# Kernel tuning notes

Measured on AMD Instinct MI355X. Metric: run time of the kernel, lower is better.

## Reference

```python
import jax, jax.numpy as jnp
import numpy as np

N_NODES = 50000
N_EDGES = 800000
IN_CH, HID_CH, OUT_CH = 512, 128, 64


def gcn_conv(x, W, b, src, dst, num_nodes):
    """PyG GCNConv: add self-loops, sym-normalize, linear, scatter-add, bias.
    x: [N, Fin], W: [Fout, Fin], b: [Fout], src/dst: [E] int."""
    loop = jnp.arange(num_nodes, dtype=src.dtype)
    src2 = jnp.concatenate([src, loop])  # [E+N]
    dst2 = jnp.concatenate([dst, loop])
    deg = jax.ops.segment_sum(jnp.ones_like(dst2, dtype=x.dtype), dst2,
                              num_segments=num_nodes)  # in-degree + 1
    d_inv_sqrt = jnp.where(deg > 0, jax.lax.rsqrt(deg), 0.0)
    norm = d_inv_sqrt[src2] * d_inv_sqrt[dst2]  # [E+N]
    h = x @ W.T  # [N, Fout]
    msg = h[src2] * norm[:, None]  # [E+N, Fout] -- dominant memory traffic
    out = jax.ops.segment_sum(msg, dst2, num_segments=num_nodes)
    return out + b


def setup_inputs() -> dict:
    key = jax.random.key(0)
    ks = jax.random.split(key, 8)
    x = jax.random.normal(ks[0], (N_NODES, IN_CH), dtype=jnp.float32)
    edge_index = jax.random.randint(ks[1], (2, N_EDGES), 0, N_NODES, dtype=jnp.int64)
    s1 = 1.0 / np.sqrt(IN_CH)
    s2 = 1.0 / np.sqrt(HID_CH)
    W1 = jax.random.normal(ks[2], (HID_CH, IN_CH), dtype=jnp.float32) * s1
    b1 = jnp.zeros((HID_CH,), dtype=jnp.float32)
    W_mu = jax.random.normal(ks[3], (OUT_CH, HID_CH), dtype=jnp.float32) * s2
    b_mu = jnp.zeros((OUT_CH,), dtype=jnp.float32)
    W_logstd = jax.random.normal(ks[4], (OUT_CH, HID_CH), dtype=jnp.float32) * s2
    b_logstd = jnp.zeros((OUT_CH,), dtype=jnp.float32)
    return {"x": x, "edge_index": edge_index, "W1": W1, "b1": b1,
            "W_mu": W_mu, "b_mu": b_mu, "W_logstd": W_logstd, "b_logstd": b_logstd}


def reference(x, edge_index, W1, b1, W_mu, b_mu, W_logstd, b_logstd):
    src, dst = edge_index[0], edge_index[1]
    n = x.shape[0]
    h = jax.nn.relu(gcn_conv(x, W1, b1, src, dst, n))
    mu = gcn_conv(h, W_mu, b_mu, src, dst, n)
    logstd = gcn_conv(h, W_logstd, b_logstd, src, dst, n)
    return (mu, logstd)
```

## Files before the change

kernel.cpp:

```cpp
#include <hip/hip_runtime.h>

constexpr int FIN = 512;
constexpr int FH  = 128;
constexpr int FO  = 64;

typedef short short8 __attribute__((ext_vector_type(8)));
typedef float f32x4 __attribute__((ext_vector_type(4)));

__device__ __forceinline__ unsigned short f2bf(float f) {
    unsigned u = __float_as_uint(f);
    u += 0x7fffu + ((u >> 16) & 1u);
    return (unsigned short)(u >> 16);
}
__device__ __forceinline__ float bf2f(unsigned short h) {
    return __uint_as_float((unsigned)h << 16);
}


__global__ void convw1_kernel(const float* __restrict__ W, unsigned short* __restrict__ Wb,
                              int n4) {
    int i = blockIdx.x * blockDim.x + threadIdx.x;
    if (i < n4) {
        float4 v = ((const float4*)W)[i];
        ushort4 p;
        p.x = f2bf(v.x); p.y = f2bf(v.y); p.z = f2bf(v.z); p.w = f2bf(v.w);
        ((ushort4*)Wb)[i] = p;
    }
}

__global__ void convw2_kernel(const float* __restrict__ Wmu, const float* __restrict__ Wlg,
                              unsigned short* __restrict__ Wh, unsigned short* __restrict__ Wl) {
    int i = blockIdx.x * blockDim.x + threadIdx.x;
    if (i < 128 * 128) {
        int r = i >> 7, c = i & 127;
        float f = (r < 64) ? Wmu[r * 128 + c] : Wlg[(r - 64) * 128 + c];
        unsigned short h = f2bf(f);
        Wh[i] = h;
        Wl[i] = f2bf(f - bf2f(h));
    }
}


__global__ void count_kernel(const int* __restrict__ dst, int* __restrict__ cnt, int E) {
    int i = blockIdx.x * blockDim.x + threadIdx.x;
    if (i < E) atomicAdd(&cnt[dst[i]], 1);
}

__global__ void dinv_kernel(const int* __restrict__ cnt, float* __restrict__ dinv, int n) {
    int i = blockIdx.x * blockDim.x + threadIdx.x;
    if (i < n) dinv[i] = rsqrtf((float)(cnt[i] + 1));
}


__global__ void scan1_kernel(const int* __restrict__ cnt, int* __restrict__ offs,
                             int* __restrict__ bsum, int n) {
    __shared__ int sdata[256];
    int t = threadIdx.x;
    int base = blockIdx.x * 1024 + t * 4;
    int4 c = make_int4(0, 0, 0, 0);
    if (base + 3 < n) {
        c = *(const int4*)(cnt + base);
    } else {
        if (base + 0 < n) c.x = cnt[base + 0];
        if (base + 1 < n) c.y = cnt[base + 1];
        if (base + 2 < n) c.z = cnt[base + 2];
        if (base + 3 < n) c.w = cnt[base + 3];
    }
    int s0 = c.x + c.y + c.z + c.w;
    sdata[t] = s0;
    __syncthreads();
    for (int off = 1; off < 256; off <<= 1) {
        int v = (t >= off) ? sdata[t - off] : 0;
        __syncthreads();
        sdata[t] += v;
        __syncthreads();
    }
    int excl = sdata[t] - s0;
    if (t == 255) bsum[blockIdx.x] = sdata[255];
    if (base + 0 < n) offs[base + 0] = excl;
    if (base + 1 < n) offs[base + 1] = excl + c.x;
    if (base + 2 < n) offs[base + 2] = excl + c.x + c.y;
    if (base + 3 < n) offs[base + 3] = excl + c.x + c.y + c.z;
}

__global__ void scan2_kernel(int* __restrict__ bsum, int nb) {
    __shared__ int sdata[256];
    int t = threadIdx.x;
    int v = (t < nb) ? bsum[t] : 0;
    sdata[t] = v;
    __syncthreads();
    for (int off = 1; off < 256; off <<= 1) {
        int u = (t >= off) ? sdata[t - off] : 0;
        __syncthreads();
        sdata[t] += u;
        __syncthreads();
    }
    if (t < nb) bsum[t] = sdata[t] - v;
}

__global__ void scan3_kernel(int* __restrict__ offs, const int* __restrict__ bsum,
                             int n, int E) {
    int i = blockIdx.x * blockDim.x + threadIdx.x;
    if (i < n) offs[i] += bsum[i >> 10];
    if (i == 0) offs[n] = E;
}


__global__ void fill_kernel(const int* __restrict__ src, const int* __restrict__ dst,
                            const float* __restrict__ dinv, const int* __restrict__ offs,
                            int* __restrict__ cursor, int2* __restrict__ esort, int E) {
    int i = blockIdx.x * blockDim.x + threadIdx.x;
    if (i < E) {
        int s = src[i];
        int d = dst[i];
        int pos = offs[d] + atomicAdd(&cursor[d], 1);
        float w = dinv[s] * dinv[d];
        esort[pos] = make_int2(s, __float_as_int(w));
    }
}


__global__ void spmm_kernel(const unsigned int* __restrict__ hin, const int* __restrict__ offs,
                            const int2* __restrict__ esort, const float* __restrict__ dinv,
                            const float* __restrict__ bias, unsigned int* __restrict__ hout,
                            int n, int relu) {
    int gid = blockIdx.x * blockDim.x + threadIdx.x;
    int node = gid >> 6;
    int lane = threadIdx.x & 63;
    if (node >= n) return;
    float di = dinv[node];
    unsigned hv = hin[(size_t)node * 64 + lane];
    float ax = di * di * __uint_as_float(hv << 16);
    float ay = di * di * __uint_as_float(hv & 0xffff0000u);
    int p = offs[node];
    int end = offs[node + 1];
    for (; p + 4 <= end; p += 4) {
        int2 e0 = esort[p + 0];
        int2 e1 = esort[p + 1];
        int2 e2 = esort[p + 2];
        int2 e3 = esort[p + 3];
        unsigned v0 = hin[(size_t)e0.x * 64 + lane];
        unsigned v1 = hin[(size_t)e1.x * 64 + lane];
        unsigned v2 = hin[(size_t)e2.x * 64 + lane];
        unsigned v3 = hin[(size_t)e3.x * 64 + lane];
        float w0 = __int_as_float(e0.y), w1 = __int_as_float(e1.y);
        float w2 = __int_as_float(e2.y), w3 = __int_as_float(e3.y);
        ax = fmaf(w0, __uint_as_float(v0 << 16), ax);
        ay = fmaf(w0, __uint_as_float(v0 & 0xffff0000u), ay);
        ax = fmaf(w1, __uint_as_float(v1 << 16), ax);
        ay = fmaf(w1, __uint_as_float(v1 & 0xffff0000u), ay);
        ax = fmaf(w2, __uint_as_float(v2 << 16), ax);
        ay = fmaf(w2, __uint_as_float(v2 & 0xffff0000u), ay);
        ax = fmaf(w3, __uint_as_float(v3 << 16), ax);
        ay = fmaf(w3, __uint_as_float(v3 & 0xffff0000u), ay);
    }
    for (; p < end; ++p) {
        int2 e = esort[p];
        unsigned v = hin[(size_t)e.x * 64 + lane];
        float w = __int_as_float(e.y);
        ax = fmaf(w, __uint_as_float(v << 16), ax);
        ay = fmaf(w, __uint_as_float(v & 0xffff0000u), ay);
    }
    if (bias) {
        float2 b = ((const float2*)bias)[lane];
        ax += b.x; ay += b.y;
    }
    if (relu) { ax = fmaxf(ax, 0.f); ay = fmaxf(ay, 0.f); }
    unsigned o = (unsigned)f2bf(ax) | ((unsigned)f2bf(ay) << 16);
    hout[(size_t)node * 64 + lane] = o;
}


__global__ __launch_bounds__(256, 3) void gemm1_kernel(
    const float* __restrict__ X, const unsigned short* __restrict__ Wb,
    unsigned short* __restrict__ out, int M) {
    __shared__ __align__(16) unsigned short As[2][64 * 64];
    __shared__ __align__(16) unsigned short Bs[2][128 * 64];

    int tid = threadIdx.x;
    int lane = tid & 63, wid = tid >> 6;
    int fr = lane & 15, fq = lane >> 4;
    int row0 = blockIdx.x * 64;

    int a_r = tid >> 4, a_kq = tid & 15;
    int b_r = tid >> 3, b_c = tid & 7;

    f32x4 acc[8] = {};
    float4 a_reg[4];
    short8 b_reg[4];

    auto issue = [&](int k0) {
        #pragma unroll
        for (int j = 0; j < 4; ++j) {
            int ar = a_r + 16 * j;
            int grow = row0 + ar; if (grow >= M) grow = M - 1;
            a_reg[j] = *(const float4*)(X + (size_t)grow * FIN + k0 + a_kq * 4);
            int br = b_r + 32 * j;
            b_reg[j] = *(const short8*)(Wb + (size_t)br * FIN + k0 + b_c * 8);
        }
    };
    auto commit = [&](int buf) {
        #pragma unroll
        for (int j = 0; j < 4; ++j) {
            int ar = a_r + 16 * j;
            ushort4 p;
            p.x = f2bf(a_reg[j].x); p.y = f2bf(a_reg[j].y);
            p.z = f2bf(a_reg[j].z); p.w = f2bf(a_reg[j].w);
            *(ushort4*)((char*)As[buf] + ar * 128 + ((a_kq * 8) ^ ((ar & 7) << 4))) = p;
            int br = b_r + 32 * j;
            *(short8*)((char*)Bs[buf] + br * 128 + ((b_c * 16) ^ ((br & 7) << 4))) = b_reg[j];
        }
    };
    auto compute = [&](int buf) {
        #pragma unroll
        for (int s = 0; s < 2; ++s) {
            int r = wid * 16 + fr;
            short8 af = *(const short8*)((const char*)As[buf] + r * 128 +
                                         ((s * 64 + fq * 16) ^ ((r & 7) << 4)));
            #pragma unroll
            for (int c = 0; c < 8; ++c) {
                int br = c * 16 + fr;
                short8 bfr = *(const short8*)((const char*)Bs[buf] + br * 128 +
                                              ((s * 64 + fq * 16) ^ ((br & 7) << 4)));
                acc[c] = __builtin_amdgcn_mfma_f32_16x16x32_bf16(af, bfr, acc[c], 0, 0, 0);
            }
        }
    };

    issue(0);
    commit(0);
    issue(64);
    __syncthreads();
    for (int kk = 0; kk < 8; ++kk) {
        compute(kk & 1);
        if (kk < 7) commit((kk + 1) & 1);
        if (kk < 6) issue((kk + 2) * 64);
        __syncthreads();
    }

    #pragma unroll
    for (int c = 0; c < 8; ++c) {
        #pragma unroll
        for (int j = 0; j < 4; ++j) {
            int row = row0 + wid * 16 + fq * 4 + j;
            if (row < M) out[(size_t)row * FH + c * 16 + fr] = f2bf(acc[c][j]);
        }
    }
}


__global__ __launch_bounds__(512) void gemm2_kernel(
    const unsigned short* __restrict__ Xb,
    const unsigned short* __restrict__ Wh, const unsigned short* __restrict__ Wl,
    float* __restrict__ outA, float* __restrict__ outB,
    const float* __restrict__ biasA, const float* __restrict__ biasB,
    int M, int nstrips) {
    __shared__ __align__(16) unsigned short WhS[128 * 128];
    __shared__ __align__(16) unsigned short WlS[128 * 128];
    int tid = threadIdx.x;

    #pragma unroll
    for (int j = 0; j < 4; ++j) {
        int f = tid + j * 512;
        int row = f >> 4;
        unsigned addr = ((unsigned)f * 16u) ^ ((unsigned)(row & 7) << 4);
        *(short8*)((char*)WhS + addr) = ((const short8*)Wh)[f];
        *(short8*)((char*)WlS + addr) = ((const short8*)Wl)[f];
    }
    __syncthreads();

    int lane = tid & 63, wid = tid >> 6;
    int fr = lane & 15, fq = lane >> 4;
    int s = blockIdx.x * 8 + wid;
    if (s >= nstrips) return;
    int row0 = s * 16;
    int arow = row0 + fr; if (arow > M - 1) arow = M - 1;
    const unsigned short* ap = Xb + (size_t)arow * FH + fq * 8;

    short8 a0 = *(const short8*)(ap + 0);
    short8 a1 = *(const short8*)(ap + 32);
    short8 a2 = *(const short8*)(ap + 64);
    short8 a3 = *(const short8*)(ap + 96);

    f32x4 acc[8] = {};

    auto proc = [&](int k0, short8 a) {
        int cb = k0 * 2 + fq * 16;
        #pragma unroll
        for (int c = 0; c < 8; ++c) {
            int lr = c * 16 + fr;
            unsigned addr = ((unsigned)(lr * 256 + cb)) ^ ((unsigned)(lr & 7) << 4);
            short8 bh = *(const short8*)((const char*)WhS + addr);
            short8 bl = *(const short8*)((const char*)WlS + addr);
            acc[c] = __builtin_amdgcn_mfma_f32_16x16x32_bf16(a, bh, acc[c], 0, 0, 0);
            acc[c] = __builtin_amdgcn_mfma_f32_16x16x32_bf16(a, bl, acc[c], 0, 0, 0);
        }
    };
    proc(0, a0);
    proc(32, a1);
    proc(64, a2);
    proc(96, a3);

    #pragma unroll
    for (int c = 0; c < 8; ++c) {
        float* outp = (c < 4) ? outA : outB;
        const float* bp = (c < 4) ? biasA : biasB;
        int col = (c & 3) * 16 + fr;
        float bv = bp[col];
        #pragma unroll
        for (int j = 0; j < 4; ++j) {
            int row = row0 + fq * 4 + j;
            if (row < M) outp[(size_t)row * FO + col] = acc[c][j] + bv;
        }
    }
}


extern "C" void kernel_launch(void* const* d_in, const int* in_sizes, int n_in,
                              void* d_out, int out_size, void* d_ws, size_t ws_size,
                              hipStream_t stream) {
    const float* x   = (const float*)d_in[0];
    const int*   ei  = (const int*)d_in[1];
    const float* W1  = (const float*)d_in[2];
    const float* b1  = (const float*)d_in[3];
    const float* Wmu = (const float*)d_in[4];
    const float* bmu = (const float*)d_in[5];
    const float* Wlg = (const float*)d_in[6];
    const float* blg = (const float*)d_in[7];

    const int n = in_sizes[0] / FIN;
    const int E = in_sizes[1] / 2;
    const int* src = ei;
    const int* dst = ei + E;
    const int nstrips = (n + 15) / 16;

    char* ws = (char*)d_ws;
    size_t off = 0;
    auto alloc = [&](size_t bytes) -> void* {
        void* p = ws + off;
        off = (off + bytes + 255) & ~((size_t)255);
        return p;
    };
    int*   cnt    = (int*)  alloc((size_t)n * 4);
    int*   offs   = (int*)  alloc((size_t)(n + 1) * 4);
    int*   cursor = (int*)  alloc((size_t)n * 4);
    int*   bsum   = (int*)  alloc(1024);
    float* dinv   = (float*)alloc((size_t)n * 4);
    int2*  esort  = (int2*) alloc((size_t)E * 8);
    unsigned short* hbf  = (unsigned short*)alloc((size_t)n * FH * 2);
    unsigned short* h1bf = (unsigned short*)alloc((size_t)n * FH * 2);
    unsigned short* ah2b = (unsigned short*)alloc((size_t)n * FH * 2);
    unsigned short* W1b = (unsigned short*)alloc((size_t)FH * FIN * 2);
    unsigned short* W2h = (unsigned short*)alloc((size_t)FH * FH * 2);
    unsigned short* W2l = (unsigned short*)alloc((size_t)FH * FH * 2);

    hipMemsetAsync(cnt, 0, (size_t)n * 4, stream);
    hipMemsetAsync(cursor, 0, (size_t)n * 4, stream);

    convw1_kernel<<<(FH * FIN / 4 + 255) / 256, 256, 0, stream>>>(W1, W1b, FH * FIN / 4);
    convw2_kernel<<<(FH * FH + 255) / 256, 256, 0, stream>>>(Wmu, Wlg, W2h, W2l);

    count_kernel<<<(E + 255) / 256, 256, 0, stream>>>(dst, cnt, E);
    dinv_kernel<<<(n + 255) / 256, 256, 0, stream>>>(cnt, dinv, n);

    int nb = (n + 1023) / 1024;
    scan1_kernel<<<nb, 256, 0, stream>>>(cnt, offs, bsum, n);
    scan2_kernel<<<1, 256, 0, stream>>>(bsum, nb);
    scan3_kernel<<<(n + 255) / 256, 256, 0, stream>>>(offs, bsum, n, E);

    fill_kernel<<<(E + 255) / 256, 256, 0, stream>>>(src, dst, dinv, offs, cursor, esort, E);

    gemm1_kernel<<<(n + 63) / 64, 256, 0, stream>>>(x, W1b, hbf, n);
    spmm_kernel<<<(n + 3) / 4, 256, 0, stream>>>(
        (const unsigned*)hbf, offs, esort, dinv, b1, (unsigned*)h1bf, n, 1);
    spmm_kernel<<<(n + 3) / 4, 256, 0, stream>>>(
        (const unsigned*)h1bf, offs, esort, dinv, nullptr, (unsigned*)ah2b, n, 0);
    float* outmu = (float*)d_out;
    float* outlg = outmu + (size_t)n * FO;
    gemm2_kernel<<<512, 512, 0, stream>>>(ah2b, W2h, W2l, outmu, outlg, bmu, blg, n, nstrips);
}
```

Measured before the change: 210.7 us.

## Fuse preprocessing kernels, keep W1 resident in LDS, widen spmm edge loads

The count and both weight-conversion kernels are merged into a single launch, and the dinv computation moves into the first scan kernel, cutting launch count and one pass over cnt. gemm1 becomes a 1024-thread block that loads all of W1 (128 KB bf16) into LDS once. Each wave then streams its own 16-row strip of X straight from global memory into registers with a software prefetch, removing per-k-step LDS staging and barriers. spmm is realigned to even edge offsets and reads pairs of edges as int4, unrolled by 8, to raise memory-level parallelism. Risks are low occupancy from the 128 KB dynamic LDS allocation and the need for the host to opt in to that much shared memory.

```diff
diff --git a/kernel.cpp b/kernel.cpp
--- a/kernel.cpp
+++ b/kernel.cpp
@@ -15,23 +15,27 @@
 __device__ __forceinline__ float bf2f(unsigned short h) {
     return __uint_as_float((unsigned)h << 16);
 }
-
-
-__global__ void convw1_kernel(const float* __restrict__ W, unsigned short* __restrict__ Wb,
-                              int n4) {
-    int i = blockIdx.x * blockDim.x + threadIdx.x;
-    if (i < n4) {
-        float4 v = ((const float4*)W)[i];
+__device__ __forceinline__ float bflo(unsigned v) { return __uint_as_float(v << 16); }
+__device__ __forceinline__ float bfhi(unsigned v) { return __uint_as_float(v & 0xffff0000u); }
+
+
+__global__ void pre_kernel(const int* __restrict__ dst, int* __restrict__ cnt, int E,
+                           const float* __restrict__ W1, unsigned short* __restrict__ W1b,
+                           const float* __restrict__ Wmu, const float* __restrict__ Wlg,
+                           unsigned short* __restrict__ Wh, unsigned short* __restrict__ Wl,
+                           int cntB) {
+    int b = blockIdx.x;
+    if (b < cntB) {
+        int i = b * 256 + threadIdx.x;
+        if (i < E) atomicAdd(&cnt[dst[i]], 1);
+    } else if (b < cntB + 64) {
+        int i = (b - cntB) * 256 + threadIdx.x;
+        float4 v = ((const float4*)W1)[i];
         ushort4 p;
         p.x = f2bf(v.x); p.y = f2bf(v.y); p.z = f2bf(v.z); p.w = f2bf(v.w);
-        ((ushort4*)Wb)[i] = p;
-    }
-}
-
-__global__ void convw2_kernel(const float* __restrict__ Wmu, const float* __restrict__ Wlg,
-                              unsigned short* __restrict__ Wh, unsigned short* __restrict__ Wl) {
-    int i = blockIdx.x * blockDim.x + threadIdx.x;
-    if (i < 128 * 128) {
+        ((ushort4*)W1b)[i] = p;
+    } else {
+        int i = (b - cntB - 64) * 256 + threadIdx.x;
         int r = i >> 7, c = i & 127;
         float f = (r < 64) ? Wmu[r * 128 + c] : Wlg[(r - 64) * 128 + c];
         unsigned short h = f2bf(f);
@@ -41,19 +45,8 @@
 }
 
 
-__global__ void count_kernel(const int* __restrict__ dst, int* __restrict__ cnt, int E) {
-    int i = blockIdx.x * blockDim.x + threadIdx.x;
-    if (i < E) atomicAdd(&cnt[dst[i]], 1);
-}
-
-__global__ void dinv_kernel(const int* __restrict__ cnt, float* __restrict__ dinv, int n) {
-    int i = blockIdx.x * blockDim.x + threadIdx.x;
-    if (i < n) dinv[i] = rsqrtf((float)(cnt[i] + 1));
-}
-
-
 __global__ void scan1_kernel(const int* __restrict__ cnt, int* __restrict__ offs,
-                             int* __restrict__ bsum, int n) {
+                             int* __restrict__ bsum, float* __restrict__ dinv, int n) {
     __shared__ int sdata[256];
     int t = threadIdx.x;
     int base = blockIdx.x * 1024 + t * 4;
@@ -66,6 +59,11 @@
         if (base + 2 < n) c.z = cnt[base + 2];
         if (base + 3 < n) c.w = cnt[base + 3];
     }
+    if (base + 0 < n) dinv[base + 0] = rsqrtf((float)(c.x + 1));
+    if (base + 1 < n) dinv[base + 1] = rsqrtf((float)(c.y + 1));
+    if (base + 2 < n) dinv[base + 2] = rsqrtf((float)(c.z + 1));
+    if (base + 3 < n) dinv[base + 3] = rsqrtf((float)(c.w + 1));
+
     int s0 = c.x + c.y + c.z + c.w;
     sdata[t] = s0;
     __syncthreads();
@@ -130,36 +128,56 @@
     if (node >= n) return;
     float di = dinv[node];
     unsigned hv = hin[(size_t)node * 64 + lane];
-    float ax = di * di * __uint_as_float(hv << 16);
-    float ay = di * di * __uint_as_float(hv & 0xffff0000u);
+    float ax = di * di * bflo(hv);
+    float ay = di * di * bfhi(hv);
     int p = offs[node];
     int end = offs[node + 1];
-    for (; p + 4 <= end; p += 4) {
-        int2 e0 = esort[p + 0];
-        int2 e1 = esort[p + 1];
-        int2 e2 = esort[p + 2];
-        int2 e3 = esort[p + 3];
-        unsigned v0 = hin[(size_t)e0.x * 64 + lane];
-        unsigned v1 = hin[(size_t)e1.x * 64 + lane];
-        unsigned v2 = hin[(size_t)e2.x * 64 + lane];
-        unsigned v3 = hin[(size_t)e3.x * 64 + lane];
-        float w0 = __int_as_float(e0.y), w1 = __int_as_float(e1.y);
-        float w2 = __int_as_float(e2.y), w3 = __int_as_float(e3.y);
-        ax = fmaf(w0, __uint_as_float(v0 << 16), ax);
-        ay = fmaf(w0, __uint_as_float(v0 & 0xffff0000u), ay);
-        ax = fmaf(w1, __uint_as_float(v1 << 16), ax);
-        ay = fmaf(w1, __uint_as_float(v1 & 0xffff0000u), ay);
-        ax = fmaf(w2, __uint_as_float(v2 << 16), ax);
-        ay = fmaf(w2, __uint_as_float(v2 & 0xffff0000u), ay);
-        ax = fmaf(w3, __uint_as_float(v3 << 16), ax);
-        ay = fmaf(w3, __uint_as_float(v3 & 0xffff0000u), ay);
-    }
-    for (; p < end; ++p) {
+    if ((p & 1) && p < end) {
         int2 e = esort[p];
         unsigned v = hin[(size_t)e.x * 64 + lane];
         float w = __int_as_float(e.y);
-        ax = fmaf(w, __uint_as_float(v << 16), ax);
-        ay = fmaf(w, __uint_as_float(v & 0xffff0000u), ay);
+        ax = fmaf(w, bflo(v), ax); ay = fmaf(w, bfhi(v), ay);
+        ++p;
+    }
+    for (; p + 8 <= end; p += 8) {
+        int4 q0 = *(const int4*)(esort + p + 0);
+        int4 q1 = *(const int4*)(esort + p + 2);
+        int4 q2 = *(const int4*)(esort + p + 4);
+        int4 q3 = *(const int4*)(esort + p + 6);
+        unsigned v0 = hin[(size_t)q0.x * 64 + lane];
+        unsigned v1 = hin[(size_t)q0.z * 64 + lane];
+        unsigned v2 = hin[(size_t)q1.x * 64 + lane];
+        unsigned v3 = hin[(size_t)q1.z * 64 + lane];
+        unsigned v4 = hin[(size_t)q2.x * 64 + lane];
+        unsigned v5 = hin[(size_t)q2.z * 64 + lane];
+        unsigned v6 = hin[(size_t)q3.x * 64 + lane];
+        unsigned v7 = hin[(size_t)q3.z * 64 + lane];
+        float w0 = __int_as_float(q0.y), w1 = __int_as_float(q0.w);
+        float w2 = __int_as_float(q1.y), w3 = __int_as_float(q1.w);
+        float w4 = __int_as_float(q2.y), w5 = __int_as_float(q2.w);
+        float w6 = __int_as_float(q3.y), w7 = __int_as_float(q3.w);
+        ax = fmaf(w0, bflo(v0), ax); ay = fmaf(w0, bfhi(v0), ay);
+        ax = fmaf(w1, bflo(v1), ax); ay = fmaf(w1, bfhi(v1), ay);
+        ax = fmaf(w2, bflo(v2), ax); ay = fmaf(w2, bfhi(v2), ay);
+        ax = fmaf(w3, bflo(v3), ax); ay = fmaf(w3, bfhi(v3), ay);
+        ax = fmaf(w4, bflo(v4), ax); ay = fmaf(w4, bfhi(v4), ay);
+        ax = fmaf(w5, bflo(v5), ax); ay = fmaf(w5, bfhi(v5), ay);
+        ax = fmaf(w6, bflo(v6), ax); ay = fmaf(w6, bfhi(v6), ay);
+        ax = fmaf(w7, bflo(v7), ax); ay = fmaf(w7, bfhi(v7), ay);
+    }
+    for (; p + 2 <= end; p += 2) {
+        int4 q = *(const int4*)(esort + p);
+        unsigned v0 = hin[(size_t)q.x * 64 + lane];
+        unsigned v1 = hin[(size_t)q.z * 64 + lane];
+        float w0 = __int_as_float(q.y), w1 = __int_as_float(q.w);
+        ax = fmaf(w0, bflo(v0), ax); ay = fmaf(w0, bfhi(v0), ay);
+        ax = fmaf(w1, bflo(v1), ax); ay = fmaf(w1, bfhi(v1), ay);
+    }
+    if (p < end) {
+        int2 e = esort[p];
+        unsigned v = hin[(size_t)e.x * 64 + lane];
+        float w = __int_as_float(e.y);
+        ax = fmaf(w, bflo(v), ax); ay = fmaf(w, bfhi(v), ay);
     }
     if (bias) {
         float2 b = ((const float2*)bias)[lane];
@@ -171,78 +189,79 @@
 }
 
 
-__global__ __launch_bounds__(256, 3) void gemm1_kernel(
+__global__ __launch_bounds__(1024, 4) void gemm1_kernel(
     const float* __restrict__ X, const unsigned short* __restrict__ Wb,
-    unsigned short* __restrict__ out, int M) {
-    __shared__ __align__(16) unsigned short As[2][64 * 64];
-    __shared__ __align__(16) unsigned short Bs[2][128 * 64];
-
+    unsigned short* __restrict__ out, int M, int nstrips) {
+    extern __shared__ __align__(16) unsigned short Bs[];
     int tid = threadIdx.x;
+
+    #pragma unroll
+    for (int j = 0; j < 8; ++j) {
+        int f = tid + j * 1024;
+        int row = f >> 6;
+        unsigned addr = ((unsigned)f << 4) ^ ((unsigned)(row & 7) << 4);
+        *(short8*)((char*)Bs + addr) = ((const short8*)Wb)[f];
+    }
+    __syncthreads();
+
     int lane = tid & 63, wid = tid >> 6;
     int fr = lane & 15, fq = lane >> 4;
-    int row0 = blockIdx.x * 64;
-
-    int a_r = tid >> 4, a_kq = tid & 15;
-    int b_r = tid >> 3, b_c = tid & 7;
+    int s = blockIdx.x * 16 + wid;
+    if (s >= nstrips) return;
+    int row0 = s * 16;
+    int arow = row0 + fr; if (arow >= M) arow = M - 1;
+    const float* ap = X + (size_t)arow * FIN + fq * 8;
 
     f32x4 acc[8] = {};
-    float4 a_reg[4];
-    short8 b_reg[4];
-
-    auto issue = [&](int k0) {
+
+    float4 c0 = *(const float4*)(ap + 0);
+    float4 c1 = *(const float4*)(ap + 4);
+    float4 c2 = *(const float4*)(ap + 32);
+    float4 c3 = *(const float4*)(ap + 36);
+
+    #pragma unroll
+    for (int kk = 0; kk < 8; ++kk) {
+        int k0 = kk * 64;
+        float4 d0 = c0, d1 = c1, d2 = c2, d3 = c3;
+        if (kk < 7) {
+            c0 = *(const float4*)(ap + k0 + 64);
+            c1 = *(const float4*)(ap + k0 + 68);
+            c2 = *(const float4*)(ap + k0 + 96);
+            c3 = *(const float4*)(ap + k0 + 100);
+        }
+        short8 af0, af1;
+        af0[0] = (short)f2bf(d0.x); af0[1] = (short)f2bf(d0.y);
+        af0[2] = (short)f2bf(d0.z); af0[3] = (short)f2bf(d0.w);
+        af0[4] = (short)f2bf(d1.x); af0[5] = (short)f2bf(d1.y);
+        af0[6] = (short)f2bf(d1.z); af0[7] = (short)f2bf(d1.w);
+        af1[0] = (short)f2bf(d2.x); af1[1] = (short)f2bf(d2.y);
+        af1[2] = (short)f2bf(d2.z); af1[3] = (short)f2bf(d2.w);
+        af1[4] = (short)f2bf(d3.x); af1[5] = (short)f2bf(d3.y);
+        af1[6] = (short)f2bf(d3.z); af1[7] = (short)f2bf(d3.w);
+
+        int cb0 = k0 * 2 + fq * 16;
+        #pragma unroll
+        for (int c = 0; c < 8; ++c) {
+            int br = c * 16 + fr;
+            short8 b0 = *(const short8*)((const char*)Bs + br * 1024 +
+                                         ((unsigned)cb0 ^ ((unsigned)(br & 7) << 4)));
+            acc[c] = __builtin_amdgcn_mfma_f32_16x16x32_bf16(af0, b0, acc[c], 0, 0, 0);
+        }
+        int cb1 = cb0 + 64;
+        #pragma unroll
+        for (int c = 0; c < 8; ++c) {
+            int br = c * 16 + fr;
+            short8 b1 = *(const short8*)((const char*)Bs + br * 1024 +
+                                         ((unsigned)cb1 ^ ((unsigned)(br & 7) << 4)));
+            acc[c] = __builtin_amdgcn_mfma_f32_16x16x32_bf16(af1, b1, acc[c], 0, 0, 0);
+        }
+    }
+
+    #pragma unroll
+    for (int c = 0; c < 8; ++c) {
         #pragma unroll
         for (int j = 0; j < 4; ++j) {
-            int ar = a_r + 16 * j;
-            int grow = row0 + ar; if (grow >= M) grow = M - 1;
-            a_reg[j] = *(const float4*)(X + (size_t)grow * FIN + k0 + a_kq * 4);
-            int br = b_r + 32 * j;
-            b_reg[j] = *(const short8*)(Wb + (size_t)br * FIN + k0 + b_c * 8);
-        }
-    };
-    auto commit = [&](int buf) {
-        #pragma unroll
-        for (int j = 0; j < 4; ++j) {
-            int ar = a_r + 16 * j;
-            ushort4 p;
-            p.x = f2bf(a_reg[j].x); p.y = f2bf(a_reg[j].y);
-            p.z = f2bf(a_reg[j].z); p.w = f2bf(a_reg[j].w);
-            *(ushort4*)((char*)As[buf] + ar * 128 + ((a_kq * 8) ^ ((ar & 7) << 4))) = p;
-            int br = b_r + 32 * j;
-            *(short8*)((char*)Bs[buf] + br * 128 + ((b_c * 16) ^ ((br & 7) << 4))) = b_reg[j];
-        }
-    };
-    auto compute = [&](int buf) {
-        #pragma unroll
-        for (int s = 0; s < 2; ++s) {
-            int r = wid * 16 + fr;
-            short8 af = *(const short8*)((const char*)As[buf] + r * 128 +
-                                         ((s * 64 + fq * 16) ^ ((r & 7) << 4)));
-            #pragma unroll
-            for (int c = 0; c < 8; ++c) {
-                int br = c * 16 + fr;
-                short8 bfr = *(const short8*)((const char*)Bs[buf] + br * 128 +
-                                              ((s * 64 + fq * 16) ^ ((br & 7) << 4)));
-                acc[c] = __builtin_amdgcn_mfma_f32_16x16x32_bf16(af, bfr, acc[c], 0, 0, 0);
-            }
-        }
-    };
-
-    issue(0);
-    commit(0);
-    issue(64);
-    __syncthreads();
-    for (int kk = 0; kk < 8; ++kk) {
-        compute(kk & 1);
-        if (kk < 7) commit((kk + 1) & 1);
-        if (kk < 6) issue((kk + 2) * 64);
-        __syncthreads();
-    }
-
-    #pragma unroll
-    for (int c = 0; c < 8; ++c) {
-        #pragma unroll
-        for (int j = 0; j < 4; ++j) {
-            int row = row0 + wid * 16 + fq * 4 + j;
+            int row = row0 + fq * 4 + j;
             if (row < M) out[(size_t)row * FH + c * 16 + fr] = f2bf(acc[c][j]);
         }
     }
@@ -357,20 +376,17 @@
     hipMemsetAsync(cnt, 0, (size_t)n * 4, stream);
     hipMemsetAsync(cursor, 0, (size_t)n * 4, stream);
 
-    convw1_kernel<<<(FH * FIN / 4 + 255) / 256, 256, 0, stream>>>(W1, W1b, FH * FIN / 4);
-    convw2_kernel<<<(FH * FH + 255) / 256, 256, 0, stream>>>(Wmu, Wlg, W2h, W2l);
-
-    count_kernel<<<(E + 255) / 256, 256, 0, stream>>>(dst, cnt, E);
-    dinv_kernel<<<(n + 255) / 256, 256, 0, stream>>>(cnt, dinv, n);
+    int cntB = (E + 255) / 256;
+    pre_kernel<<<cntB + 128, 256, 0, stream>>>(dst, cnt, E, W1, W1b, Wmu, Wlg, W2h, W2l, cntB);
 
     int nb = (n + 1023) / 1024;
-    scan1_kernel<<<nb, 256, 0, stream>>>(cnt, offs, bsum, n);
+    scan1_kernel<<<nb, 256, 0, stream>>>(cnt, offs, bsum, dinv, n);
     scan2_kernel<<<1, 256, 0, stream>>>(bsum, nb);
     scan3_kernel<<<(n + 255) / 256, 256, 0, stream>>>(offs, bsum, n, E);
 
     fill_kernel<<<(E + 255) / 256, 256, 0, stream>>>(src, dst, dinv, offs, cursor, esort, E);
 
-    gemm1_kernel<<<(n + 63) / 64, 256, 0, stream>>>(x, W1b, hbf, n);
+    gemm1_kernel<<<(nstrips + 15) / 16, 1024, 128 * 1024, stream>>>(x, W1b, hbf, n, nstrips);
     spmm_kernel<<<(n + 3) / 4, 256, 0, stream>>>(
         (const unsigned*)hbf, offs, esort, dinv, b1, (unsigned*)h1bf, n, 1);
     spmm_kernel<<<(n + 3) / 4, 256, 0, stream>>>(
```

Result: faster. 197.7 us (-6.2%).
